# Performance work log

Measured on AMD Instinct MI355X. Metric: run time of the kernel, lower is better.

## Reference

```python
import jax, jax.numpy as jnp
import numpy as np

EPS = 1e-5

def _layernorm(x, gamma, beta):
    # normalize over last (channel) axis, per point
    mu = jnp.mean(x, axis=-1, keepdims=True)
    var = jnp.mean(jnp.square(x - mu), axis=-1, keepdims=True)
    return (x - mu) * jax.lax.rsqrt(var + EPS) * gamma + beta

def setup_inputs() -> dict:
    key = jax.random.key(0)
    ks = jax.random.split(key, 12)
    B, N, C, F = 32, 4096, 3, 1024
    points = jax.random.normal(ks[0], (B, N, C), dtype=jnp.float32)
    mask = jax.random.randint(ks[1], (B, 1, N), 0, 2, dtype=jnp.int32)
    s = 0.05
    return {
        "points": points,
        "mask": mask,
        "w1": jax.random.normal(ks[2], (128, C), dtype=jnp.float32) * s,      # conv1 (no bias)
        "g1": jnp.ones((128,), jnp.float32),                                   # norm1 gamma
        "be1": jnp.zeros((128,), jnp.float32),                                 # norm1 beta
        "w2": jax.random.normal(ks[3], (256, 128), dtype=jnp.float32) * s,     # conv2
        "b2": jax.random.normal(ks[4], (256,), dtype=jnp.float32) * s,
        "w3": jax.random.normal(ks[5], (512, 512), dtype=jnp.float32) * s,     # conv3 (no bias)
        "g2": jnp.ones((512,), jnp.float32),                                   # norm2 gamma
        "be2": jnp.zeros((512,), jnp.float32),                                 # norm2 beta
        "w4": jax.random.normal(ks[6], (F, 512), dtype=jnp.float32) * s,       # conv4
        "b4": jax.random.normal(ks[7], (F,), dtype=jnp.float32) * s,
    }

def reference(points, mask, w1, g1, be1, w2, b2, w3, g2, be2, w4, b4):
    # points: [B, N, C]; mask: [B, 1, N]
    vis = (mask[:, 0, :] != 0).astype(points.dtype)[..., None]  # [B, N, 1]
    # conv1 (1x1, no bias) as point-wise matmul
    h0 = jnp.einsum('bnc,kc->bnk', points, w1)                  # [B, N, 128]
    # masked LayerNorm: LN is per-point over channels, so compute densely and zero invisible points
    h1 = _layernorm(h0, g1, be1) * vis
    h2 = jax.nn.relu(h1)
    h3 = jnp.einsum('bnk,ok->bno', h2, w2) + b2                 # [B, N, 256]
    gmax = jnp.max(h3, axis=1, keepdims=True)                   # [B, 1, 256]
    dist = jnp.concatenate([jnp.broadcast_to(gmax, h3.shape), h3], axis=-1)  # [B, N, 512]
    h4 = jnp.einsum('bno,po->bnp', dist, w3)                    # [B, N, 512]
    h5 = _layernorm(h4, g2, be2) * vis
    h6 = jax.nn.relu(h5)
    h7 = jnp.einsum('bnp,fp->bnf', h6, w4) + b4                 # [B, N, F]
    return jnp.max(h7, axis=1)                                  # [B, F]
```

## Files before the change

kernel.cpp:

```cpp
#include <hip/hip_runtime.h>
#include <stdint.h>

#define LN_EPS 1e-5f

static __device__ __forceinline__ unsigned short f2bf_bits(float f) {
  union { float f; unsigned u; } v; v.f = f;
  unsigned r = v.u + 0x7FFFu + ((v.u >> 16) & 1u);
  return (unsigned short)(r >> 16);
}
static __device__ __forceinline__ float bf2f(unsigned short h) {
  union { unsigned u; float f; } v; v.u = ((unsigned)h) << 16;
  return v.f;
}

typedef __bf16 bf16x8 __attribute__((ext_vector_type(8)));
typedef float floatx4 __attribute__((ext_vector_type(4)));

typedef __attribute__((address_space(1))) unsigned int* gas_ptr;
typedef __attribute__((address_space(3))) unsigned int* las_ptr;
static __device__ __forceinline__ void async_cp16(const void* g, void* l) {
  __builtin_amdgcn_global_load_lds((gas_ptr)g, (las_ptr)l, 16, 0, 0);
}

__global__ __launch_bounds__(256) void perm_kernel(
    const int* __restrict__ mask, int* __restrict__ newrow, int* __restrict__ cnt) {
  const int b = blockIdx.x, t = threadIdx.x;
  const int base = b * 4096 + t * 16;
  int v[16]; int s = 0;
#pragma unroll
  for (int i = 0; i < 16; ++i) { v[i] = (mask[base + i] != 0); s += v[i]; }
  const int lane = t & 63, wv = t >> 6;
  int scan = s;
  for (int o = 1; o < 64; o <<= 1) { int x = __shfl_up(scan, o); if (lane >= o) scan += x; }
  __shared__ int wsum[4], woff[4], stotal;
  if (lane == 63) wsum[wv] = scan;
  __syncthreads();
  if (t == 0) { int a = 0; for (int k = 0; k < 4; ++k) { woff[k] = a; a += wsum[k]; } stotal = a; cnt[b] = a; }
  __syncthreads();
  const int excl = scan - s + woff[wv];
  const int total = stotal;
  int run = 0;
#pragma unroll
  for (int i = 0; i < 16; ++i) {
    const int pos = t * 16 + i;
    const int visBefore = excl + run;
    newrow[b * 4096 + pos] = v[i] ? visBefore : total + (pos - visBefore);
    run += v[i];
  }
}

__global__ __launch_bounds__(256) void conv1_ln_kernel(
    const float* __restrict__ points, const int* __restrict__ mask,
    const float* __restrict__ w1, const float* __restrict__ g1,
    const float* __restrict__ be1, unsigned short* __restrict__ h2,
    const int* __restrict__ newrow, const int* __restrict__ cnt,
    const float* __restrict__ w2, const float* __restrict__ w3,
    const float* __restrict__ w4, unsigned short* __restrict__ w2b,
    unsigned short* __restrict__ w3Rb, unsigned short* __restrict__ w4b) {
  if (blockIdx.x >= 32768) {
    int idx = (blockIdx.x - 32768) * 256 + threadIdx.x;
    if (idx < 32768) {
      w2b[idx] = f2bf_bits(w2[idx]);
    } else if (idx < 32768 + 131072) {
      int t = idx - 32768;
      int p = t >> 8, k = t & 255;
      w3Rb[t] = f2bf_bits(w3[p * 512 + 256 + k]);
    } else {
      int t = idx - 163840;
      w4b[t] = f2bf_bits(w4[t]);
    }
    return;
  }
  const int lane = threadIdx.x & 63;
  const int wv = threadIdx.x >> 6;
  const size_t p = (size_t)blockIdx.x * 4 + wv;
  const int dest = newrow[p];
  const int ceilv = (cnt[p >> 12] + 127) & ~127;
  if (dest >= ceilv) return;
  const float x0 = points[p * 3 + 0];
  const float x1 = points[p * 3 + 1];
  const float x2 = points[p * 3 + 2];
  const int c0 = lane * 2, c1 = c0 + 1;
  float h00 = w1[c0 * 3] * x0 + w1[c0 * 3 + 1] * x1 + w1[c0 * 3 + 2] * x2;
  float h01 = w1[c1 * 3] * x0 + w1[c1 * 3 + 1] * x1 + w1[c1 * 3 + 2] * x2;
  float s = h00 + h01;
  for (int o = 32; o; o >>= 1) s += __shfl_xor(s, o);
  const float mu = s * (1.f / 128.f);
  const float d0 = h00 - mu, d1 = h01 - mu;
  float q = d0 * d0 + d1 * d1;
  for (int o = 32; o; o >>= 1) q += __shfl_xor(q, o);
  const float rs = rsqrtf(q * (1.f / 128.f) + LN_EPS);
  const bool vis = (mask[p] != 0);
  const float y0 = vis ? fmaxf(d0 * rs * g1[c0] + be1[c0], 0.f) : 0.f;
  const float y1 = vis ? fmaxf(d1 * rs * g1[c1] + be1[c1], 0.f) : 0.f;
  union { unsigned u; unsigned short s2[2]; } pk;
  pk.s2[0] = f2bf_bits(y0);
  pk.s2[1] = f2bf_bits(y1);
  const size_t prow = (p & ~(size_t)4095) + (size_t)dest;
  ((unsigned*)h2)[prow * 64 + lane] = pk.u;
}

template <int EPI, int NCT>
__global__ __launch_bounds__(256) void gemm_bt(
    const unsigned short* __restrict__ A, const unsigned short* __restrict__ Bw,
    void* __restrict__ outp, float* __restrict__ outp2,
    const float* __restrict__ extra, const int* __restrict__ cnt,
    int M, int N, int K) {
  __shared__ __align__(16) char smA[2][128 * 64];
  __shared__ __align__(16) char smB[2][128 * 64];
  __shared__ float lmax[2][128];

  const int tid = threadIdx.x;
  const int lane = tid & 63;
  const int w = tid >> 6;
  const int wm = w >> 1, wn = w & 1;

  const int gid = blockIdx.x;
  const int xcd = gid & 7;
  const int slot = gid >> 3;
  const int rowsPerXcd = (M >> 7) >> 3;
  const int rowTile = xcd * rowsPerXcd + slot / NCT;
  const int colTile = slot % NCT;
  const size_t rowBase = (size_t)rowTile * 128;
  const int colBase = colTile * 128;

  const int cntb = cnt[rowBase >> 12];
  const int rb = (int)(rowBase & 4095);
  if (rb >= cntb) {
    if (EPI == 1) return;
    if (EPI == 2) {
      if (tid < 128) outp2[(size_t)rowTile * N + colBase + tid] = 0.f;
      return;
    }
    if (EPI == 3) {
      if (tid < 128) outp2[(size_t)rowTile * N + colBase + tid] = extra[colBase + tid];
      return;
    }
  }

  floatx4 acc[4][4];
  const floatx4 zero = {0.f, 0.f, 0.f, 0.f};
#pragma unroll
  for (int i = 0; i < 4; ++i)
#pragma unroll
    for (int j = 0; j < 4; ++j) acc[i][j] = zero;

  const int rSub = lane >> 2;
  const int cb16 = (lane & 3) * 16;
  const size_t Kb = (size_t)K * 2;
  const char* gA = (const char*)A + (rowBase + (size_t)(w * 32 + rSub)) * Kb + cb16;
  const char* gB = (const char*)Bw + ((size_t)colBase + (size_t)(w * 32 + rSub)) * Kb + cb16;
  char* lA0 = smA[0] + w * 2048;
  char* lA1 = smA[1] + w * 2048;
  char* lB0 = smB[0] + w * 2048;
  char* lB1 = smB[1] + w * 2048;
  const size_t skip16 = 16 * Kb;

  const int fm = lane & 15, fq = lane >> 4;
  const int fOff = fm * 64 + fq * 16;
  const char* pa0 = smA[0] + wm * 64 * 64 + fOff;
  const char* pa1 = smA[1] + wm * 64 * 64 + fOff;
  const char* pb0 = smB[0] + wn * 64 * 64 + fOff;
  const char* pb1 = smB[1] + wn * 64 * 64 + fOff;

  for (int k0 = 0; k0 < K; k0 += 64) {
    async_cp16(gA, lA0);
    async_cp16(gA + skip16, lA0 + 1024);
    async_cp16(gA + 64, lA1);
    async_cp16(gA + 64 + skip16, lA1 + 1024);
    async_cp16(gB, lB0);
    async_cp16(gB + skip16, lB0 + 1024);
    async_cp16(gB + 64, lB1);
    async_cp16(gB + 64 + skip16, lB1 + 1024);
    gA += 128; gB += 128;
    __syncthreads();
    bf16x8 af0[4], bg0[4], af1[4], bg1[4];
#pragma unroll
    for (int i = 0; i < 4; ++i) af0[i] = *(const bf16x8*)(pa0 + i * 16 * 64);
#pragma unroll
    for (int j = 0; j < 4; ++j) bg0[j] = *(const bf16x8*)(pb0 + j * 16 * 64);
#pragma unroll
    for (int i = 0; i < 4; ++i)
#pragma unroll
      for (int j = 0; j < 4; ++j)
        acc[i][j] = __builtin_amdgcn_mfma_f32_16x16x32_bf16(af0[i], bg0[j], acc[i][j], 0, 0, 0);
#pragma unroll
    for (int i = 0; i < 4; ++i) af1[i] = *(const bf16x8*)(pa1 + i * 16 * 64);
#pragma unroll
    for (int j = 0; j < 4; ++j) bg1[j] = *(const bf16x8*)(pb1 + j * 16 * 64);
#pragma unroll
    for (int i = 0; i < 4; ++i)
#pragma unroll
      for (int j = 0; j < 4; ++j)
        acc[i][j] = __builtin_amdgcn_mfma_f32_16x16x32_bf16(af1[i], bg1[j], acc[i][j], 0, 0, 0);
    __syncthreads();
  }

  float m4[4] = {-1e30f, -1e30f, -1e30f, -1e30f};

  if (EPI == 1 || EPI == 3) {
    unsigned short* O = (unsigned short*)outp;
#pragma unroll
    for (int j = 0; j < 4; ++j) {
      const int col = colBase + wn * 64 + j * 16 + fm;
      const float ex = (EPI == 1) ? extra[(rowBase >> 12) * (size_t)N + col] : extra[col];
#pragma unroll
      for (int i = 0; i < 4; ++i) {
        const size_t row0 = rowBase + wm * 64 + i * 16 + fq * 4;
#pragma unroll
        for (int r = 0; r < 4; ++r) {
          const float v = acc[i][j][r] + ex;
          if (EPI == 3) m4[j] = fmaxf(m4[j], v);
          O[(row0 + r) * (size_t)N + col] = f2bf_bits(v);
        }
      }
    }
  } else {
#pragma unroll
    for (int j = 0; j < 4; ++j) {
#pragma unroll
      for (int i = 0; i < 4; ++i)
#pragma unroll
        for (int r = 0; r < 4; ++r) m4[j] = fmaxf(m4[j], acc[i][j][r]);
    }
  }

  if (EPI == 2 || EPI == 3) {
#pragma unroll
    for (int j = 0; j < 4; ++j) {
      m4[j] = fmaxf(m4[j], __shfl_xor(m4[j], 16));
      m4[j] = fmaxf(m4[j], __shfl_xor(m4[j], 32));
    }
    const float sel = (fq == 0) ? m4[0] : (fq == 1) ? m4[1] : (fq == 2) ? m4[2] : m4[3];
    lmax[wm][wn * 64 + fq * 16 + fm] = sel;
    __syncthreads();
    if (tid < 128) {
      const float v = fmaxf(lmax[0][tid], lmax[1][tid]);
      outp2[(size_t)rowTile * N + colBase + tid] = v;
    }
  }
}

__global__ __launch_bounds__(256) void gmax_cvec_kernel(
    const float* __restrict__ pg, const float* __restrict__ w3,
    float* __restrict__ cvec) {
  __shared__ float gm[256];
  const int b = blockIdx.x, t = threadIdx.x;
  float m = -1e30f;
  for (int s = 0; s < 32; ++s) m = fmaxf(m, pg[((size_t)b * 32 + s) * 256 + t]);
  gm[t] = m;
  __syncthreads();
#pragma unroll
  for (int half = 0; half < 2; ++half) {
    const int p = half * 256 + t;
    const float* wr = w3 + (size_t)p * 512;
    float s = 0.f;
    for (int c = 0; c < 256; ++c) s += wr[c] * gm[c];
    cvec[b * 512 + p] = s;
  }
}

__global__ __launch_bounds__(256) void ln2_kernel(
    unsigned short* __restrict__ h46, const int* __restrict__ cnt,
    const float* __restrict__ g2, const float* __restrict__ be2) {
  const int lane = threadIdx.x & 63;
  const int wv = threadIdx.x >> 6;
  const size_t p = (size_t)blockIdx.x * 4 + wv;
  const int cb = cnt[p >> 12];
  const int pin = (int)(p & 4095);
  const int ceilv = (cb + 127) & ~127;
  if (pin >= ceilv) return;
  unsigned short* row = h46 + p * 512;
  const int c0 = lane * 8;
  if (pin >= cb) {
    const uint4 z = {0, 0, 0, 0};
    *(uint4*)(row + c0) = z;
    return;
  }
  union { uint4 v; unsigned short s[8]; } in;
  in.v = *(const uint4*)(row + c0);
  float f[8];
  float s = 0.f;
#pragma unroll
  for (int k = 0; k < 8; ++k) { f[k] = bf2f(in.s[k]); s += f[k]; }
  for (int o = 32; o; o >>= 1) s += __shfl_xor(s, o);
  const float mu = s * (1.f / 512.f);
  float q = 0.f;
#pragma unroll
  for (int k = 0; k < 8; ++k) { const float d = f[k] - mu; q += d * d; }
  for (int o = 32; o; o >>= 1) q += __shfl_xor(q, o);
  const float rs = rsqrtf(q * (1.f / 512.f) + LN_EPS);
  union { uint4 v; unsigned short s[8]; } outv;
#pragma unroll
  for (int k = 0; k < 8; ++k) {
    const float y = fmaxf((f[k] - mu) * rs * g2[c0 + k] + be2[c0 + k], 0.f);
    outv.s[k] = f2bf_bits(y);
  }
  *(uint4*)(row + c0) = outv.v;
}

__global__ __launch_bounds__(256) void final_kernel(
    const float* __restrict__ pmax, const float* __restrict__ b4,
    float* __restrict__ out) {
  const int idx = blockIdx.x * 256 + threadIdx.x;
  const int b = idx >> 10, f = idx & 1023;
  float m = -1e30f;
  for (int r = 0; r < 32; ++r) m = fmaxf(m, pmax[((size_t)(b * 32 + r)) * 1024 + f]);
  out[idx] = m + b4[f];
}

extern "C" void kernel_launch(void* const* d_in, const int* in_sizes, int n_in,
                              void* d_out, int out_size, void* d_ws, size_t ws_size,
                              hipStream_t stream) {
  const float* points = (const float*)d_in[0];
  const int* mask = (const int*)d_in[1];
  const float* w1 = (const float*)d_in[2];
  const float* g1 = (const float*)d_in[3];
  const float* be1 = (const float*)d_in[4];
  const float* w2 = (const float*)d_in[5];
  const float* b2 = (const float*)d_in[6];
  const float* w3 = (const float*)d_in[7];
  const float* g2 = (const float*)d_in[8];
  const float* be2 = (const float*)d_in[9];
  const float* w4 = (const float*)d_in[10];
  const float* b4 = (const float*)d_in[11];
  float* out = (float*)d_out;
  char* ws = (char*)d_ws;

  const size_t OFF_H46 = 0;
  const size_t OFF_H2 = 0;
  const size_t OFF_H3 = 134217728;
  const size_t OFF_W2B = OFF_H3 + 67108864;
  const size_t OFF_W3RB = OFF_W2B + 65536;
  const size_t OFF_W4B = OFF_W3RB + 262144;
  const size_t OFF_PG = OFF_W4B + 1048576;
  const size_t OFF_CVEC = OFF_PG + 1048576;
  const size_t OFF_PMAX = OFF_CVEC + 65536;
  const size_t OFF_CNT = OFF_PMAX + 4194304;
  const size_t OFF_NEWROW = OFF_CNT + 4096;

  unsigned short* h2 = (unsigned short*)(ws + OFF_H2);
  unsigned short* h3 = (unsigned short*)(ws + OFF_H3);
  unsigned short* h46 = (unsigned short*)(ws + OFF_H46);
  unsigned short* w2b = (unsigned short*)(ws + OFF_W2B);
  unsigned short* w3Rb = (unsigned short*)(ws + OFF_W3RB);
  unsigned short* w4b = (unsigned short*)(ws + OFF_W4B);
  float* pg = (float*)(ws + OFF_PG);
  float* cvecp = (float*)(ws + OFF_CVEC);
  float* pmaxp = (float*)(ws + OFF_PMAX);
  int* cntp = (int*)(ws + OFF_CNT);
  int* newrow = (int*)(ws + OFF_NEWROW);

  perm_kernel<<<32, 256, 0, stream>>>(mask, newrow, cntp);
  conv1_ln_kernel<<<32768 + 2688, 256, 0, stream>>>(points, mask, w1, g1, be1, h2,
                                                    newrow, cntp, w2, w3, w4, w2b, w3Rb, w4b);
  gemm_bt<3, 2><<<2048, 256, 0, stream>>>(h2, w2b, (void*)h3, pg, b2, cntp, 131072, 256, 128);
  gmax_cvec_kernel<<<32, 256, 0, stream>>>(pg, w3, cvecp);
  gemm_bt<1, 4><<<4096, 256, 0, stream>>>(h3, w3Rb, (void*)h46, nullptr, cvecp, cntp, 131072, 512, 256);
  ln2_kernel<<<32768, 256, 0, stream>>>(h46, cntp, g2, be2);
  gemm_bt<2, 8><<<8192, 256, 0, stream>>>(h46, w4b, nullptr, pmaxp, nullptr, cntp, 131072, 1024, 512);
  final_kernel<<<128, 256, 0, stream>>>(pmaxp, b4, out);
}
```

Before: 287.3 us.

## Fuse LayerNorm2 into conv3 GEMM with full-row tiles; read weights directly from global

Conv3 becomes a GEMM whose 32-row tiles cover all 512 output channels, so LayerNorm2 and ReLU are applied in the epilogue using cross-wave sum and sum-of-squares reductions. This removes the separate ln2 pass that re-read and re-wrote h46. The conv3 and conv4 GEMMs now load B fragments straight from global memory instead of staging them through LDS, and the shared template is split into specialized kernels. The fused kernel computes variance in one pass as E[x²]−mu², which is less numerically stable. Its smaller row tiles also mean weights are reused less per block.

```diff
diff --git a/kernel.cpp b/kernel.cpp
--- a/kernel.cpp
+++ b/kernel.cpp
@@ -100,10 +100,9 @@
   ((unsigned*)h2)[prow * 64 + lane] = pk.u;
 }
 
-template <int EPI, int NCT>
-__global__ __launch_bounds__(256) void gemm_bt(
+__global__ __launch_bounds__(256) void gemm2_kernel(
     const unsigned short* __restrict__ A, const unsigned short* __restrict__ Bw,
-    void* __restrict__ outp, float* __restrict__ outp2,
+    unsigned short* __restrict__ outp, float* __restrict__ outp2,
     const float* __restrict__ extra, const int* __restrict__ cnt,
     int M, int N, int K) {
   __shared__ __align__(16) char smA[2][128 * 64];
@@ -115,6 +114,7 @@
   const int w = tid >> 6;
   const int wm = w >> 1, wn = w & 1;
 
+  const int NCT = 2;
   const int gid = blockIdx.x;
   const int xcd = gid & 7;
   const int slot = gid >> 3;
@@ -127,15 +127,8 @@
   const int cntb = cnt[rowBase >> 12];
   const int rb = (int)(rowBase & 4095);
   if (rb >= cntb) {
-    if (EPI == 1) return;
-    if (EPI == 2) {
-      if (tid < 128) outp2[(size_t)rowTile * N + colBase + tid] = 0.f;
-      return;
-    }
-    if (EPI == 3) {
-      if (tid < 128) outp2[(size_t)rowTile * N + colBase + tid] = extra[colBase + tid];
-      return;
-    }
+    if (tid < 128) outp2[(size_t)rowTile * N + colBase + tid] = extra[colBase + tid];
+    return;
   }
 
   floatx4 acc[4][4];
@@ -197,47 +190,32 @@
   }
 
   float m4[4] = {-1e30f, -1e30f, -1e30f, -1e30f};
-
-  if (EPI == 1 || EPI == 3) {
-    unsigned short* O = (unsigned short*)outp;
-#pragma unroll
-    for (int j = 0; j < 4; ++j) {
-      const int col = colBase + wn * 64 + j * 16 + fm;
-      const float ex = (EPI == 1) ? extra[(rowBase >> 12) * (size_t)N + col] : extra[col];
-#pragma unroll
-      for (int i = 0; i < 4; ++i) {
-        const size_t row0 = rowBase + wm * 64 + i * 16 + fq * 4;
-#pragma unroll
-        for (int r = 0; r < 4; ++r) {
-          const float v = acc[i][j][r] + ex;
-          if (EPI == 3) m4[j] = fmaxf(m4[j], v);
-          O[(row0 + r) * (size_t)N + col] = f2bf_bits(v);
-        }
+#pragma unroll
+  for (int j = 0; j < 4; ++j) {
+    const int col = colBase + wn * 64 + j * 16 + fm;
+    const float ex = extra[col];
+#pragma unroll
+    for (int i = 0; i < 4; ++i) {
+      const size_t row0 = rowBase + wm * 64 + i * 16 + fq * 4;
+#pragma unroll
+      for (int r = 0; r < 4; ++r) {
+        const float v = acc[i][j][r] + ex;
+        m4[j] = fmaxf(m4[j], v);
+        outp[(row0 + r) * (size_t)N + col] = f2bf_bits(v);
       }
     }
-  } else {
-#pragma unroll
-    for (int j = 0; j < 4; ++j) {
-#pragma unroll
-      for (int i = 0; i < 4; ++i)
-#pragma unroll
-        for (int r = 0; r < 4; ++r) m4[j] = fmaxf(m4[j], acc[i][j][r]);
-    }
-  }
-
-  if (EPI == 2 || EPI == 3) {
-#pragma unroll
-    for (int j = 0; j < 4; ++j) {
-      m4[j] = fmaxf(m4[j], __shfl_xor(m4[j], 16));
-      m4[j] = fmaxf(m4[j], __shfl_xor(m4[j], 32));
-    }
-    const float sel = (fq == 0) ? m4[0] : (fq == 1) ? m4[1] : (fq == 2) ? m4[2] : m4[3];
-    lmax[wm][wn * 64 + fq * 16 + fm] = sel;
-    __syncthreads();
-    if (tid < 128) {
-      const float v = fmaxf(lmax[0][tid], lmax[1][tid]);
-      outp2[(size_t)rowTile * N + colBase + tid] = v;
-    }
+  }
+#pragma unroll
+  for (int j = 0; j < 4; ++j) {
+    m4[j] = fmaxf(m4[j], __shfl_xor(m4[j], 16));
+    m4[j] = fmaxf(m4[j], __shfl_xor(m4[j], 32));
+  }
+  const float sel = (fq == 0) ? m4[0] : (fq == 1) ? m4[1] : (fq == 2) ? m4[2] : m4[3];
+  lmax[wm][wn * 64 + fq * 16 + fm] = sel;
+  __syncthreads();
+  if (tid < 128) {
+    const float v = fmaxf(lmax[0][tid], lmax[1][tid]);
+    outp2[(size_t)rowTile * N + colBase + tid] = v;
   }
 }
 
@@ -260,43 +238,243 @@
   }
 }
 
-__global__ __launch_bounds__(256) void ln2_kernel(
-    unsigned short* __restrict__ h46, const int* __restrict__ cnt,
-    const float* __restrict__ g2, const float* __restrict__ be2) {
-  const int lane = threadIdx.x & 63;
-  const int wv = threadIdx.x >> 6;
-  const size_t p = (size_t)blockIdx.x * 4 + wv;
-  const int cb = cnt[p >> 12];
-  const int pin = (int)(p & 4095);
-  const int ceilv = (cb + 127) & ~127;
-  if (pin >= ceilv) return;
-  unsigned short* row = h46 + p * 512;
-  const int c0 = lane * 8;
-  if (pin >= cb) {
-    const uint4 z = {0, 0, 0, 0};
-    *(uint4*)(row + c0) = z;
+__global__ __launch_bounds__(256) void gemm3_ln_kernel(
+    const unsigned short* __restrict__ A, const unsigned short* __restrict__ Bw,
+    unsigned short* __restrict__ outp, const float* __restrict__ cvec,
+    const int* __restrict__ cnt, const float* __restrict__ g2,
+    const float* __restrict__ be2) {
+  __shared__ __align__(16) char smA[2][32 * 64];
+  __shared__ float sSum[4][32], sSq[4][32], sMu[32], sRs[32];
+
+  const int tid = threadIdx.x;
+  const int lane = tid & 63;
+  const int w = tid >> 6;
+
+  const int gid = blockIdx.x;
+  const int rowTile = (gid & 7) * 512 + (gid >> 3);
+  const size_t rowBase = (size_t)rowTile * 32;
+  const int batch = (int)(rowBase >> 12);
+  const int rb = (int)(rowBase & 4095);
+  const int cntb = cnt[batch];
+  const int ceil128 = (cntb + 127) & ~127;
+  if (rb >= ceil128) return;
+  if (rb >= cntb) {
+    uint4 z = {0, 0, 0, 0};
+    uint4* O = (uint4*)(outp + rowBase * 512);
+    for (int t = tid; t < 2048; t += 256) O[t] = z;
     return;
   }
-  union { uint4 v; unsigned short s[8]; } in;
-  in.v = *(const uint4*)(row + c0);
-  float f[8];
-  float s = 0.f;
-#pragma unroll
-  for (int k = 0; k < 8; ++k) { f[k] = bf2f(in.s[k]); s += f[k]; }
-  for (int o = 32; o; o >>= 1) s += __shfl_xor(s, o);
-  const float mu = s * (1.f / 512.f);
-  float q = 0.f;
-#pragma unroll
-  for (int k = 0; k < 8; ++k) { const float d = f[k] - mu; q += d * d; }
-  for (int o = 32; o; o >>= 1) q += __shfl_xor(q, o);
-  const float rs = rsqrtf(q * (1.f / 512.f) + LN_EPS);
-  union { uint4 v; unsigned short s[8]; } outv;
-#pragma unroll
-  for (int k = 0; k < 8; ++k) {
-    const float y = fmaxf((f[k] - mu) * rs * g2[c0 + k] + be2[c0 + k], 0.f);
-    outv.s[k] = f2bf_bits(y);
-  }
-  *(uint4*)(row + c0) = outv.v;
+
+  floatx4 acc[2][8];
+  const floatx4 zero = {0.f, 0.f, 0.f, 0.f};
+#pragma unroll
+  for (int i = 0; i < 2; ++i)
+#pragma unroll
+    for (int j = 0; j < 8; ++j) acc[i][j] = zero;
+
+  const int rSub = lane >> 2;
+  const int cb16 = (lane & 3) * 16;
+  const int p_st = w >> 1, h_st = w & 1;
+  const char* gA = (const char*)A + (rowBase + (size_t)(h_st * 16 + rSub)) * 512 + p_st * 64 + cb16;
+  char* lA = smA[p_st] + h_st * 1024;
+
+  const int fm = lane & 15, fq = lane >> 4;
+  const char* pB = (const char*)Bw + (size_t)(w * 128 + fm) * 512 + fq * 16;
+
+  const char* pa0 = smA[0] + fm * 64 + fq * 16;
+  const char* pa1 = smA[1] + fm * 64 + fq * 16;
+
+  int koff = 0;
+  for (int it = 0; it < 4; ++it) {
+    async_cp16(gA, lA);
+    gA += 128;
+    bf16x8 bg0[8], bg1[8];
+#pragma unroll
+    for (int j = 0; j < 8; ++j) bg0[j] = *(const bf16x8*)(pB + j * 8192 + koff);
+#pragma unroll
+    for (int j = 0; j < 8; ++j) bg1[j] = *(const bf16x8*)(pB + j * 8192 + koff + 64);
+    __syncthreads();
+    bf16x8 af0[2], af1[2];
+#pragma unroll
+    for (int i = 0; i < 2; ++i) af0[i] = *(const bf16x8*)(pa0 + i * 16 * 64);
+#pragma unroll
+    for (int i = 0; i < 2; ++i) af1[i] = *(const bf16x8*)(pa1 + i * 16 * 64);
+#pragma unroll
+    for (int i = 0; i < 2; ++i)
+#pragma unroll
+      for (int j = 0; j < 8; ++j)
+        acc[i][j] = __builtin_amdgcn_mfma_f32_16x16x32_bf16(af0[i], bg0[j], acc[i][j], 0, 0, 0);
+#pragma unroll
+    for (int i = 0; i < 2; ++i)
+#pragma unroll
+      for (int j = 0; j < 8; ++j)
+        acc[i][j] = __builtin_amdgcn_mfma_f32_16x16x32_bf16(af1[i], bg1[j], acc[i][j], 0, 0, 0);
+    koff += 128;
+    __syncthreads();
+  }
+
+  float ex[8];
+#pragma unroll
+  for (int j = 0; j < 8; ++j) ex[j] = cvec[batch * 512 + w * 128 + j * 16 + fm];
+  float sS[2][4], sQ[2][4];
+#pragma unroll
+  for (int i = 0; i < 2; ++i)
+#pragma unroll
+    for (int r = 0; r < 4; ++r) {
+      float s = 0.f, q = 0.f;
+#pragma unroll
+      for (int j = 0; j < 8; ++j) {
+        const float v = acc[i][j][r] + ex[j];
+        acc[i][j][r] = v;
+        s += v; q += v * v;
+      }
+#pragma unroll
+      for (int off = 1; off < 16; off <<= 1) {
+        s += __shfl_xor(s, off);
+        q += __shfl_xor(q, off);
+      }
+      sS[i][r] = s; sQ[i][r] = q;
+    }
+  if (fm == 0) {
+#pragma unroll
+    for (int i = 0; i < 2; ++i)
+#pragma unroll
+      for (int r = 0; r < 4; ++r) {
+        const int row = i * 16 + fq * 4 + r;
+        sSum[w][row] = sS[i][r];
+        sSq[w][row] = sQ[i][r];
+      }
+  }
+  __syncthreads();
+  if (tid < 32) {
+    const float S = sSum[0][tid] + sSum[1][tid] + sSum[2][tid] + sSum[3][tid];
+    const float Q = sSq[0][tid] + sSq[1][tid] + sSq[2][tid] + sSq[3][tid];
+    const float mu = S * (1.f / 512.f);
+    sMu[tid] = mu;
+    sRs[tid] = rsqrtf(Q * (1.f / 512.f) - mu * mu + LN_EPS);
+  }
+  __syncthreads();
+
+  float gj[8], bj[8];
+#pragma unroll
+  for (int j = 0; j < 8; ++j) {
+    const int col = w * 128 + j * 16 + fm;
+    gj[j] = g2[col]; bj[j] = be2[col];
+  }
+#pragma unroll
+  for (int i = 0; i < 2; ++i)
+#pragma unroll
+    for (int r = 0; r < 4; ++r) {
+      const int row = i * 16 + fq * 4 + r;
+      const float mu = sMu[row], rs = sRs[row];
+      const bool live = (rb + row) < cntb;
+#pragma unroll
+      for (int j = 0; j < 8; ++j) {
+        const int col = w * 128 + j * 16 + fm;
+        float y = live ? fmaxf((acc[i][j][r] - mu) * rs * gj[j] + bj[j], 0.f) : 0.f;
+        outp[(rowBase + row) * 512 + col] = f2bf_bits(y);
+      }
+    }
+}
+
+__global__ __launch_bounds__(256) void gemm4_kernel(
+    const unsigned short* __restrict__ A, const unsigned short* __restrict__ Bw,
+    float* __restrict__ outp2, const int* __restrict__ cnt, int M, int N, int K) {
+  __shared__ __align__(16) char smA[2][128 * 64];
+  __shared__ float lmax[2][128];
+
+  const int tid = threadIdx.x;
+  const int lane = tid & 63;
+  const int w = tid >> 6;
+  const int wm = w >> 1, wn = w & 1;
+
+  const int NCT = 8;
+  const int gid = blockIdx.x;
+  const int xcd = gid & 7;
+  const int slot = gid >> 3;
+  const int rowsPerXcd = (M >> 7) >> 3;
+  const int rowTile = xcd * rowsPerXcd + slot / NCT;
+  const int colTile = slot % NCT;
+  const size_t rowBase = (size_t)rowTile * 128;
+  const int colBase = colTile * 128;
+
+  const int cntb = cnt[rowBase >> 12];
+  const int rb = (int)(rowBase & 4095);
+  if (rb >= cntb) {
+    if (tid < 128) outp2[(size_t)rowTile * N + colBase + tid] = 0.f;
+    return;
+  }
+
+  floatx4 acc[4][4];
+  const floatx4 zero = {0.f, 0.f, 0.f, 0.f};
+#pragma unroll
+  for (int i = 0; i < 4; ++i)
+#pragma unroll
+    for (int j = 0; j < 4; ++j) acc[i][j] = zero;
+
+  const int rSub = lane >> 2;
+  const int cb16 = (lane & 3) * 16;
+  const size_t Kb = (size_t)K * 2;
+  const char* gA = (const char*)A + (rowBase + (size_t)(w * 32 + rSub)) * Kb + cb16;
+  char* lA0 = smA[0] + w * 2048;
+  char* lA1 = smA[1] + w * 2048;
+  const size_t skip16 = 16 * Kb;
+
+  const int fm = lane & 15, fq = lane >> 4;
+  const int fOff = fm * 64 + fq * 16;
+  const char* pa0 = smA[0] + wm * 64 * 64 + fOff;
+  const char* pa1 = smA[1] + wm * 64 * 64 + fOff;
+  const char* pB = (const char*)Bw + ((size_t)colBase + wn * 64 + fm) * Kb + fq * 16;
+
+  size_t koff = 0;
+  for (int k0 = 0; k0 < K; k0 += 64) {
+    async_cp16(gA, lA0);
+    async_cp16(gA + skip16, lA0 + 1024);
+    async_cp16(gA + 64, lA1);
+    async_cp16(gA + 64 + skip16, lA1 + 1024);
+    gA += 128;
+    bf16x8 bg0[4], bg1[4];
+#pragma unroll
+    for (int j = 0; j < 4; ++j) bg0[j] = *(const bf16x8*)(pB + (size_t)j * 16 * Kb + koff);
+#pragma unroll
+    for (int j = 0; j < 4; ++j) bg1[j] = *(const bf16x8*)(pB + (size_t)j * 16 * Kb + koff + 64);
+    __syncthreads();
+    bf16x8 af0[4], af1[4];
+#pragma unroll
+    for (int i = 0; i < 4; ++i) af0[i] = *(const bf16x8*)(pa0 + i * 16 * 64);
+#pragma unroll
+    for (int i = 0; i < 4; ++i) af1[i] = *(const bf16x8*)(pa1 + i * 16 * 64);
+#pragma unroll
+    for (int i = 0; i < 4; ++i)
+#pragma unroll
+      for (int j = 0; j < 4; ++j)
+        acc[i][j] = __builtin_amdgcn_mfma_f32_16x16x32_bf16(af0[i], bg0[j], acc[i][j], 0, 0, 0);
+#pragma unroll
+    for (int i = 0; i < 4; ++i)
+#pragma unroll
+      for (int j = 0; j < 4; ++j)
+        acc[i][j] = __builtin_amdgcn_mfma_f32_16x16x32_bf16(af1[i], bg1[j], acc[i][j], 0, 0, 0);
+    koff += 128;
+    __syncthreads();
+  }
+
+  float m4[4] = {-1e30f, -1e30f, -1e30f, -1e30f};
+#pragma unroll
+  for (int j = 0; j < 4; ++j) {
+#pragma unroll
+    for (int i = 0; i < 4; ++i)
+#pragma unroll
+      for (int r = 0; r < 4; ++r) m4[j] = fmaxf(m4[j], acc[i][j][r]);
+    m4[j] = fmaxf(m4[j], __shfl_xor(m4[j], 16));
+    m4[j] = fmaxf(m4[j], __shfl_xor(m4[j], 32));
+  }
+  const float sel = (fq == 0) ? m4[0] : (fq == 1) ? m4[1] : (fq == 2) ? m4[2] : m4[3];
+  lmax[wm][wn * 64 + fq * 16 + fm] = sel;
+  __syncthreads();
+  if (tid < 128) {
+    const float v = fmaxf(lmax[0][tid], lmax[1][tid]);
+    outp2[(size_t)rowTile * N + colBase + tid] = v;
+  }
 }
 
 __global__ __launch_bounds__(256) void final_kernel(
@@ -354,10 +532,9 @@
   perm_kernel<<<32, 256, 0, stream>>>(mask, newrow, cntp);
   conv1_ln_kernel<<<32768 + 2688, 256, 0, stream>>>(points, mask, w1, g1, be1, h2,
                                                     newrow, cntp, w2, w3, w4, w2b, w3Rb, w4b);
-  gemm_bt<3, 2><<<2048, 256, 0, stream>>>(h2, w2b, (void*)h3, pg, b2, cntp, 131072, 256, 128);
+  gemm2_kernel<<<2048, 256, 0, stream>>>(h2, w2b, h3, pg, b2, cntp, 131072, 256, 128);
   gmax_cvec_kernel<<<32, 256, 0, stream>>>(pg, w3, cvecp);
-  gemm_bt<1, 4><<<4096, 256, 0, stream>>>(h3, w3Rb, (void*)h46, nullptr, cvecp, cntp, 131072, 512, 256);
-  ln2_kernel<<<32768, 256, 0, stream>>>(h46, cntp, g2, be2);
-  gemm_bt<2, 8><<<8192, 256, 0, stream>>>(h46, w4b, nullptr, pmaxp, nullptr, cntp, 131072, 1024, 512);
+  gemm3_ln_kernel<<<4096, 256, 0, stream>>>(h3, w3Rb, h46, cvecp, cntp, g2, be2);
+  gemm4_kernel<<<8192, 256, 0, stream>>>(h46, w4b, pmaxp, cntp, 131072, 1024, 512);
   final_kernel<<<128, 256, 0, stream>>>(pmaxp, b4, out);
 }
```

After: 377.6 us. 1.31x slower.
